# Kernel optimization log

Hardware: AMD Instinct MI355X
Metric: run time of the kernel (lower is better)

The kernel has to match this reference:

```python
import jax, jax.numpy as jnp
import numpy as np

TEMPERATURE = 8.0  # sqrt(head_dim=64)

def setup_inputs() -> dict:
    key = jax.random.key(0)
    kq, kk, kv = jax.random.split(key, 3)
    shape = (4, 16, 2048, 64)  # [B, H, S, D]
    q = jax.random.normal(kq, shape, dtype=jnp.float32)
    k = jax.random.normal(kk, shape, dtype=jnp.float32)
    v = jax.random.normal(kv, shape, dtype=jnp.float32)
    return {"q": q, "k": k, "v": v}

def reference(q, k, v):
    # attn = softmax((q / temperature) @ k^T); dropout is identity (p effectively 0 / eval mode)
    scores = jnp.einsum("bhqd,bhkd->bhqk", q / TEMPERATURE, k)  # [B,H,S,S]
    attn = jax.nn.softmax(scores, axis=-1)
    output = jnp.einsum("bhqk,bhkd->bhqd", attn, v)  # [B,H,S,D]
    return (output, attn)
```

## Files before the change

### kernel.cpp

```cpp
#include <hip/hip_runtime.h>


#define S 2048
#define D 64
#define BH 64
#define TEMP_INV 0.125f

using short8  = __attribute__((ext_vector_type(8))) short;
using floatx4 = __attribute__((ext_vector_type(4))) float;

static __device__ __forceinline__ short bf(float f) {
  union { float f; unsigned u; } c; c.f = f;
  unsigned r = c.u + 0x7fffu + ((c.u >> 16) & 1u);
  return (short)(r >> 16);
}

constexpr int KS  = 72;
constexpr int VTS = 40;
constexpr int PS  = 36;

__global__ __launch_bounds__(256)
void sdpa_kernel(const float* __restrict__ q, const float* __restrict__ k,
                 const float* __restrict__ v, float* __restrict__ out) {
  __shared__ __align__(16) short Kt[32 * KS];
  __shared__ __align__(16) short VT[64 * VTS];
  __shared__ __align__(16) float Pl[4][16 * PS];

  const int g    = blockIdx.x;
  const int xcd  = g & 7;
  const int s    = g >> 3;
  const int head = xcd + 8 * (s >> 5);
  const int qt   = s & 31;

  const int tid  = threadIdx.x;
  const int wave = tid >> 6;
  const int lane = tid & 63;
  const int quad = lane >> 4;
  const int l16  = lane & 15;

  const size_t headOff = (size_t)head * S * D;
  const int    qrow0   = qt * 64 + wave * 16;

  const float* qr = q + headOff + (size_t)(qrow0 + l16) * D;
  short8 qa, qb;
#pragma unroll
  for (int j = 0; j < 8; ++j) {
    qa[j] = bf(qr[quad * 8 + j] * TEMP_INV);
    qb[j] = bf(qr[32 + quad * 8 + j] * TEMP_INV);
  }

  const float* kg = k + headOff;
  const float* vg = v + headOff;

  float l[4] = {0.f, 0.f, 0.f, 0.f};
  for (int jt = 0; jt < 64; ++jt) {
    __syncthreads();
    {
      const float4* src = (const float4*)(kg + (size_t)jt * 32 * D);
#pragma unroll
      for (int i = tid; i < 512; i += 256) {
        float4 f = src[i];
        int key = i >> 4, d4 = (i & 15) * 4;
        short4 sv; sv.x = bf(f.x); sv.y = bf(f.y); sv.z = bf(f.z); sv.w = bf(f.w);
        *(short4*)&Kt[key * KS + d4] = sv;
      }
    }
    __syncthreads();
#pragma unroll
    for (int h = 0; h < 2; ++h) {
      short8 b0 = *(const short8*)&Kt[(h * 16 + l16) * KS + quad * 8];
      short8 b1 = *(const short8*)&Kt[(h * 16 + l16) * KS + 32 + quad * 8];
      floatx4 acc = {0.f, 0.f, 0.f, 0.f};
      acc = __builtin_amdgcn_mfma_f32_16x16x32_bf16(qa, b0, acc, 0, 0, 0);
      acc = __builtin_amdgcn_mfma_f32_16x16x32_bf16(qb, b1, acc, 0, 0, 0);
#pragma unroll
      for (int r = 0; r < 4; ++r) l[r] += __expf(acc[r]);
    }
  }
#pragma unroll
  for (int off = 1; off < 16; off <<= 1) {
#pragma unroll
    for (int r = 0; r < 4; ++r) l[r] += __shfl_xor(l[r], off);
  }
  float rcp[4];
#pragma unroll
  for (int r = 0; r < 4; ++r) rcp[r] = 1.0f / l[r];

  floatx4 accO[4];
#pragma unroll
  for (int d0 = 0; d0 < 4; ++d0) accO[d0] = floatx4{0.f, 0.f, 0.f, 0.f};

  float* attn = out + (size_t)BH * S * D;
  float* arow = attn + (size_t)head * S * S + (size_t)qrow0 * S;

  for (int jt = 0; jt < 64; ++jt) {
    __syncthreads();
    {
      const float4* src = (const float4*)(kg + (size_t)jt * 32 * D);
#pragma unroll
      for (int i = tid; i < 512; i += 256) {
        float4 f = src[i];
        int key = i >> 4, d4 = (i & 15) * 4;
        short4 sv; sv.x = bf(f.x); sv.y = bf(f.y); sv.z = bf(f.z); sv.w = bf(f.w);
        *(short4*)&Kt[key * KS + d4] = sv;
      }
      const float4* vsrc = (const float4*)(vg + (size_t)jt * 32 * D);
#pragma unroll
      for (int i = tid; i < 512; i += 256) {
        float4 f = vsrc[i];
        int key = i >> 4, d4 = (i & 15) * 4;
        VT[(d4 + 0) * VTS + key] = bf(f.x);
        VT[(d4 + 1) * VTS + key] = bf(f.y);
        VT[(d4 + 2) * VTS + key] = bf(f.z);
        VT[(d4 + 3) * VTS + key] = bf(f.w);
      }
    }
    __syncthreads();

    floatx4 sc[2];
#pragma unroll
    for (int h = 0; h < 2; ++h) {
      short8 b0 = *(const short8*)&Kt[(h * 16 + l16) * KS + quad * 8];
      short8 b1 = *(const short8*)&Kt[(h * 16 + l16) * KS + 32 + quad * 8];
      floatx4 acc = {0.f, 0.f, 0.f, 0.f};
      acc = __builtin_amdgcn_mfma_f32_16x16x32_bf16(qa, b0, acc, 0, 0, 0);
      acc = __builtin_amdgcn_mfma_f32_16x16x32_bf16(qb, b1, acc, 0, 0, 0);
      sc[h] = acc;
    }

#pragma unroll
    for (int h = 0; h < 2; ++h) {
#pragma unroll
      for (int r = 0; r < 4; ++r) {
        float p = __expf(sc[h][r]) * rcp[r];
        arow[(size_t)(quad * 4 + r) * S + jt * 32 + h * 16 + l16] = p;
        Pl[wave][(quad * 4 + r) * PS + h * 16 + l16] = p;
      }
    }

    float4 pa = *(const float4*)&Pl[wave][l16 * PS + quad * 8];
    float4 pb = *(const float4*)&Pl[wave][l16 * PS + quad * 8 + 4];
    short8 pf;
    pf[0] = bf(pa.x); pf[1] = bf(pa.y); pf[2] = bf(pa.z); pf[3] = bf(pa.w);
    pf[4] = bf(pb.x); pf[5] = bf(pb.y); pf[6] = bf(pb.z); pf[7] = bf(pb.w);

#pragma unroll
    for (int d0 = 0; d0 < 4; ++d0) {
      short8 vf = *(const short8*)&VT[(d0 * 16 + l16) * VTS + quad * 8];
      accO[d0] = __builtin_amdgcn_mfma_f32_16x16x32_bf16(pf, vf, accO[d0], 0, 0, 0);
    }
  }

  float* orow = out + headOff;
#pragma unroll
  for (int d0 = 0; d0 < 4; ++d0) {
#pragma unroll
    for (int r = 0; r < 4; ++r) {
      orow[(size_t)(qrow0 + quad * 4 + r) * D + d0 * 16 + l16] = accO[d0][r];
    }
  }
}

extern "C" void kernel_launch(void* const* d_in, const int* in_sizes, int n_in,
                              void* d_out, int out_size, void* d_ws, size_t ws_size,
                              hipStream_t stream) {
  const float* q = (const float*)d_in[0];
  const float* k = (const float*)d_in[1];
  const float* v = (const float*)d_in[2];
  float* out = (float*)d_out;
  sdpa_kernel<<<2048, 256, 0, stream>>>(q, k, v, out);
}
```

Before: 1.678 ms.

## Pre-convert K and transposed V to bf16 in workspace, read directly from global

Result: no change. 1.662 ms (-1.0%).

```diff
diff --git a/kernel.cpp b/kernel.cpp
--- a/kernel.cpp
+++ b/kernel.cpp
@@ -15,16 +15,158 @@
   return (short)(r >> 16);
 }
 
+__global__ __launch_bounds__(256)
+void convert_bf16(const float* __restrict__ src, short* __restrict__ dst, int n4) {
+  int i = blockIdx.x * 256 + threadIdx.x;
+  if (i >= n4) return;
+  float4 f = ((const float4*)src)[i];
+  short4 o; o.x = bf(f.x); o.y = bf(f.y); o.z = bf(f.z); o.w = bf(f.w);
+  ((short4*)dst)[i] = o;
+}
+
+__global__ __launch_bounds__(256)
+void transpose_v_bf16(const float* __restrict__ v, short* __restrict__ vt) {
+  __shared__ short T[64][72];
+  const int head = blockIdx.x >> 5;
+  const int s0   = (blockIdx.x & 31) * 64;
+  const float4* src = (const float4*)(v + ((size_t)head * S + s0) * D);
+  for (int i = threadIdx.x; i < 1024; i += 256) {
+    int srow = i >> 4, d4 = (i & 15) * 4;
+    float4 f = src[i];
+    T[d4 + 0][srow] = bf(f.x);
+    T[d4 + 1][srow] = bf(f.y);
+    T[d4 + 2][srow] = bf(f.z);
+    T[d4 + 3][srow] = bf(f.w);
+  }
+  __syncthreads();
+  short* dst = vt + (size_t)head * D * S + s0;
+  for (int i = threadIdx.x; i < 1024; i += 256) {
+    int d = i >> 4, c4 = (i & 15) * 4;
+    short4 o; o.x = T[d][c4]; o.y = T[d][c4 + 1]; o.z = T[d][c4 + 2]; o.w = T[d][c4 + 3];
+    *(short4*)&dst[(size_t)d * S + c4] = o;
+  }
+}
+
+constexpr int PS = 36;
+
+__global__ __launch_bounds__(256)
+void sdpa_fast(const float* __restrict__ q, const short* __restrict__ kb,
+               const short* __restrict__ vtb, float* __restrict__ out) {
+  __shared__ float Pl[4][16 * PS];
+
+  const int g    = blockIdx.x;
+  const int xcd  = g & 7;
+  const int s_   = g >> 3;
+  const int head = xcd + 8 * (s_ >> 5);
+  const int qt   = s_ & 31;
+
+  const int tid  = threadIdx.x;
+  const int wave = tid >> 6;
+  const int lane = tid & 63;
+  const int quad = lane >> 4;
+  const int l16  = lane & 15;
+
+  const size_t headOff = (size_t)head * S * D;
+  const int    qrow0   = qt * 64 + wave * 16;
+
+  const float* qr = q + headOff + (size_t)(qrow0 + l16) * D;
+  short8 qa, qb;
+#pragma unroll
+  for (int j = 0; j < 8; ++j) {
+    qa[j] = bf(qr[quad * 8 + j] * TEMP_INV);
+    qb[j] = bf(qr[32 + quad * 8 + j] * TEMP_INV);
+  }
+
+  const short* kh = kb  + headOff;
+  const short* vh = vtb + headOff;
+
+  float l[4] = {0.f, 0.f, 0.f, 0.f};
+  for (int jt = 0; jt < 32; ++jt) {
+#pragma unroll
+    for (int h = 0; h < 4; ++h) {
+      const short* kr = kh + (size_t)(jt * 64 + h * 16 + l16) * D + quad * 8;
+      short8 b0 = *(const short8*)kr;
+      short8 b1 = *(const short8*)(kr + 32);
+      floatx4 acc = {0.f, 0.f, 0.f, 0.f};
+      acc = __builtin_amdgcn_mfma_f32_16x16x32_bf16(qa, b0, acc, 0, 0, 0);
+      acc = __builtin_amdgcn_mfma_f32_16x16x32_bf16(qb, b1, acc, 0, 0, 0);
+#pragma unroll
+      for (int r = 0; r < 4; ++r) l[r] += __expf(acc[r]);
+    }
+  }
+#pragma unroll
+  for (int off = 1; off < 16; off <<= 1) {
+#pragma unroll
+    for (int r = 0; r < 4; ++r) l[r] += __shfl_xor(l[r], off);
+  }
+  float rcp[4];
+#pragma unroll
+  for (int r = 0; r < 4; ++r) rcp[r] = 1.0f / l[r];
+
+  floatx4 accO[4];
+#pragma unroll
+  for (int d0 = 0; d0 < 4; ++d0) accO[d0] = floatx4{0.f, 0.f, 0.f, 0.f};
+
+  float* attn = out + (size_t)BH * S * D;
+  float* arow = attn + (size_t)head * S * S + (size_t)qrow0 * S;
+
+  for (int jt = 0; jt < 64; ++jt) {
+    floatx4 sc[2];
+#pragma unroll
+    for (int h = 0; h < 2; ++h) {
+      const short* kr = kh + (size_t)(jt * 32 + h * 16 + l16) * D + quad * 8;
+      short8 b0 = *(const short8*)kr;
+      short8 b1 = *(const short8*)(kr + 32);
+      floatx4 acc = {0.f, 0.f, 0.f, 0.f};
+      acc = __builtin_amdgcn_mfma_f32_16x16x32_bf16(qa, b0, acc, 0, 0, 0);
+      acc = __builtin_amdgcn_mfma_f32_16x16x32_bf16(qb, b1, acc, 0, 0, 0);
+      sc[h] = acc;
+    }
+
+#pragma unroll
+    for (int h = 0; h < 2; ++h) {
+#pragma unroll
+      for (int r = 0; r < 4; ++r) {
+        float p = __expf(sc[h][r]) * rcp[r];
+        __builtin_nontemporal_store(
+            p, &arow[(size_t)(quad * 4 + r) * S + jt * 32 + h * 16 + l16]);
+        Pl[wave][(quad * 4 + r) * PS + h * 16 + l16] = p;
+      }
+    }
+
+    float4 pa = *(const float4*)&Pl[wave][l16 * PS + quad * 8];
+    float4 pb = *(const float4*)&Pl[wave][l16 * PS + quad * 8 + 4];
+    short8 pf;
+    pf[0] = bf(pa.x); pf[1] = bf(pa.y); pf[2] = bf(pa.z); pf[3] = bf(pa.w);
+    pf[4] = bf(pb.x); pf[5] = bf(pb.y); pf[6] = bf(pb.z); pf[7] = bf(pb.w);
+
+#pragma unroll
+    for (int d0 = 0; d0 < 4; ++d0) {
+      const short* vr = vh + (size_t)(d0 * 16 + l16) * S + jt * 32 + quad * 8;
+      short8 vf = *(const short8*)vr;
+      accO[d0] = __builtin_amdgcn_mfma_f32_16x16x32_bf16(pf, vf, accO[d0], 0, 0, 0);
+    }
+  }
+
+  float* orow = out + headOff;
+#pragma unroll
+  for (int d0 = 0; d0 < 4; ++d0) {
+#pragma unroll
+    for (int r = 0; r < 4; ++r) {
+      orow[(size_t)(qrow0 + quad * 4 + r) * D + d0 * 16 + l16] = accO[d0][r];
+    }
+  }
+}
+
 constexpr int KS  = 72;
 constexpr int VTS = 40;
-constexpr int PS  = 36;
 
 __global__ __launch_bounds__(256)
-void sdpa_kernel(const float* __restrict__ q, const float* __restrict__ k,
-                 const float* __restrict__ v, float* __restrict__ out) {
+void sdpa_kernel_ref(const float* __restrict__ q, const float* __restrict__ k,
+                     const float* __restrict__ v, float* __restrict__ out) {
   __shared__ __align__(16) short Kt[32 * KS];
   __shared__ __align__(16) short VT[64 * VTS];
-  __shared__ __align__(16) float Pl[4][16 * PS];
+  __shared__ __align__(16) float Pl2[4][16 * PS];
 
   const int g    = blockIdx.x;
   const int xcd  = g & 7;
@@ -134,12 +276,12 @@
       for (int r = 0; r < 4; ++r) {
         float p = __expf(sc[h][r]) * rcp[r];
         arow[(size_t)(quad * 4 + r) * S + jt * 32 + h * 16 + l16] = p;
-        Pl[wave][(quad * 4 + r) * PS + h * 16 + l16] = p;
-      }
-    }
-
-    float4 pa = *(const float4*)&Pl[wave][l16 * PS + quad * 8];
-    float4 pb = *(const float4*)&Pl[wave][l16 * PS + quad * 8 + 4];
+        Pl2[wave][(quad * 4 + r) * PS + h * 16 + l16] = p;
+      }
+    }
+
+    float4 pa = *(const float4*)&Pl2[wave][l16 * PS + quad * 8];
+    float4 pb = *(const float4*)&Pl2[wave][l16 * PS + quad * 8 + 4];
     short8 pf;
     pf[0] = bf(pa.x); pf[1] = bf(pa.y); pf[2] = bf(pa.z); pf[3] = bf(pa.w);
     pf[4] = bf(pb.x); pf[5] = bf(pb.y); pf[6] = bf(pb.z); pf[7] = bf(pb.w);
@@ -168,5 +310,17 @@
   const float* k = (const float*)d_in[1];
   const float* v = (const float*)d_in[2];
   float* out = (float*)d_out;
-  sdpa_kernel<<<2048, 256, 0, stream>>>(q, k, v, out);
-}
+
+  constexpr size_t ELEMS   = (size_t)BH * S * D;
+  constexpr size_t WS_NEED = 2 * ELEMS * sizeof(short);
+
+  if (d_ws != nullptr && ws_size >= WS_NEED) {
+    short* kb  = (short*)d_ws;
+    short* vtb = kb + ELEMS;
+    convert_bf16<<<(int)(ELEMS / 4 / 256), 256, 0, stream>>>(k, kb, (int)(ELEMS / 4));
+    transpose_v_bf16<<<2048, 256, 0, stream>>>(v, vtb);
+    sdpa_fast<<<2048, 256, 0, stream>>>(q, kb, vtb, out);
+  } else {
+    sdpa_kernel_ref<<<2048, 256, 0, stream>>>(q, k, v, out);
+  }
+}
```
